# Kernel optimization log

Hardware: AMD Instinct MI355X
Metric: run time of the kernel (lower is better)

The kernel has to match this reference:

```python
import jax, jax.numpy as jnp
import numpy as np

N_NODES = 100000
N_EDGES = 1600000
D_IN, D_H, D_OUT = 256, 128, 128


def setup_inputs() -> dict:
    key = jax.random.key(0)
    ks = jax.random.split(key, 8)
    x = jax.random.normal(ks[0], (N_NODES, D_IN), dtype=jnp.float32)
    edge_index = jax.random.randint(ks[1], (2, N_EDGES), 0, N_NODES, dtype=jnp.int64)
    def glorot(k, fan_in, fan_out):
        s = jnp.sqrt(6.0 / (fan_in + fan_out))
        return jax.random.uniform(k, (fan_in, fan_out), jnp.float32, -s, s)
    W1 = glorot(ks[2], D_IN, D_H)
    b1 = jnp.zeros((D_H,), jnp.float32)
    W2 = glorot(ks[3], D_H, D_H)
    b2 = jnp.zeros((D_H,), jnp.float32)
    W3 = glorot(ks[4], D_H, D_OUT)
    b3 = jnp.zeros((D_OUT,), jnp.float32)
    return {"x": x, "edge_index": edge_index,
            "W1": W1, "b1": b1, "W2": W2, "b2": b2, "W3": W3, "b3": b3}


def _gcn_norm(edge_index, n_nodes):
    # PyG GCNConv: add self-loops, symmetric normalization D^-1/2 (A+I) D^-1/2
    loop = jnp.arange(n_nodes, dtype=edge_index.dtype)
    src = jnp.concatenate([edge_index[0], loop])  # source j
    dst = jnp.concatenate([edge_index[1], loop])  # target i
    deg = jax.ops.segment_sum(jnp.ones_like(dst, dtype=jnp.float32), dst,
                              num_segments=n_nodes)
    dinv = jnp.where(deg > 0, jax.lax.rsqrt(deg), 0.0)
    norm = dinv[src] * dinv[dst]  # [E+N]
    return src, dst, norm


def _gcn_conv(h, W, b, src, dst, norm, n_nodes):
    h = h @ W                                   # [N, d_out] transform first
    msg = h[src] * norm[:, None]                # gather + edge-weight
    out = jax.ops.segment_sum(msg, dst, num_segments=n_nodes)  # scatter-add
    return out + b


def reference(x, edge_index, W1, b1, W2, b2, W3, b3):
    n = x.shape[0]
    src, dst, norm = _gcn_norm(edge_index, n)
    h = jax.nn.relu(_gcn_conv(x, W1, b1, src, dst, norm, n))
    h = jax.nn.relu(_gcn_conv(h, W2, b2, src, dst, norm, n))
    return _gcn_conv(h, W3, b3, src, dst, norm, n)
```

## Files before the change

### kernel.cpp

```cpp
#include <hip/hip_runtime.h>
#include <hip/hip_fp16.h>
#include <math.h>


#define N_NODES 100000
#define N_EDGES 1600000
#define SLOT    56
#define NWIN    6

typedef _Float16 f16x8 __attribute__((ext_vector_type(8)));
typedef float    f32x4 __attribute__((ext_vector_type(4)));


__global__ __launch_bounds__(256) void k_init(int* __restrict__ csr, int total,
                                              int* __restrict__ cnt, int n,
                                              unsigned int* __restrict__ phz,
                                              unsigned int* __restrict__ phz2) {
    int i = blockIdx.x * 256 + threadIdx.x;
    if (i < total) csr[i] = N_NODES;
    if (i < n) cnt[i] = 0;
    if (i < 64) { phz[i] = 0; phz2[i] = 0; }
}

__global__ __launch_bounds__(256) void k_dinv(const int* __restrict__ cnt, float* __restrict__ dinv, int n) {
    int i = blockIdx.x * 256 + threadIdx.x;
    if (i < n) dinv[i] = rsqrtf((float)(cnt[i] + 1));
    else if (i == n) dinv[i] = 0.f;
}

__global__ __launch_bounds__(256) void k_wpack(const float* __restrict__ W, _Float16* __restrict__ Wpk, int K) {
    int j = blockIdx.x * 256 + threadIdx.x;
    if (j < K * 128) {
        int i  = j & 7;
        int l  = (j >> 3) & 63;
        int tc = (j >> 9) & 7;
        int c  = j >> 12;
        int col = tc * 16 + (l & 15);
        int k   = c * 32 + (l >> 4) * 8 + i;
        float w = W[(size_t)k * 128 + col];
        _Float16 h = (_Float16)w;
        Wpk[j] = h;
        Wpk[(size_t)K * 128 + j] = (_Float16)(w - (float)h);
    }
}


template <int K>
__global__ __launch_bounds__(256) void k_gemm1_fill(const float* __restrict__ X,
                                                    const _Float16* __restrict__ Wpk,
                                                    _Float16* __restrict__ Y, int n,
                                                    const int* __restrict__ src, const int* __restrict__ dst,
                                                    int* __restrict__ cnt, int* __restrict__ csr,
                                                    int E, int lo, int hi, int gemm_b0, int gemm_nb) {
    constexpr int NS = K / 64;
    __shared__ float sX[64 * 64];
    if ((int)blockIdx.x >= gemm_nb) {
        int e = (blockIdx.x - gemm_nb) * 256 + threadIdx.x;
        if (e < E) {
            int d = dst[e];
            if (d >= lo && d < hi) {
                int p = atomicAdd(&cnt[d], 1);
                csr[d * SLOT + p] = src[e];
            }
        }
        return;
    }
    const int t    = threadIdx.x;
    const int wave = t >> 6;
    const int lane = t & 63;
    const int lrow = lane & 15;
    const int kgrp = lane >> 4;
    const int row0 = (gemm_b0 + blockIdx.x) * 64;
    const int R    = wave * 16 + lrow;
    const _Float16* __restrict__ Wlo = Wpk + (size_t)K * 128;

    const int gsl = t & 15;
    const int rb  = t >> 4;
    const int r0 = rb, r1 = rb + 16, r2 = rb + 32, r3 = rb + 48;
    const int gc0 = ((gsl & 8) + ((gsl & 7) ^ (r0 & 7))) << 2;
    const int gc1 = ((gsl & 8) + ((gsl & 7) ^ (r1 & 7))) << 2;
    const int gc2 = ((gsl & 8) + ((gsl & 7) ^ (r2 & 7))) << 2;
    const int gc3 = ((gsl & 8) + ((gsl & 7) ^ (r3 & 7))) << 2;
    const bool ok0 = row0 + r0 < n, ok1 = row0 + r1 < n;
    const bool ok2 = row0 + r2 < n, ok3 = row0 + r3 < n;
    const float* __restrict__ xr0 = X + (size_t)(row0 + r0) * K;
    const float* __restrict__ xr1 = X + (size_t)(row0 + r1) * K;
    const float* __restrict__ xr2 = X + (size_t)(row0 + r2) * K;
    const float* __restrict__ xr3 = X + (size_t)(row0 + r3) * K;

    f32x4 acc[8];
    #pragma unroll
    for (int i = 0; i < 8; ++i) acc[i] = (f32x4){0.f, 0.f, 0.f, 0.f};

    const float4 z4 = make_float4(0.f, 0.f, 0.f, 0.f);
    float4 rv0 = ok0 ? *(const float4*)&xr0[gc0] : z4;
    float4 rv1 = ok1 ? *(const float4*)&xr1[gc1] : z4;
    float4 rv2 = ok2 ? *(const float4*)&xr2[gc2] : z4;
    float4 rv3 = ok3 ? *(const float4*)&xr3[gc3] : z4;
    *(float4*)&sX[(r0 * 16 + gsl) * 4] = rv0;
    *(float4*)&sX[(r1 * 16 + gsl) * 4] = rv1;
    *(float4*)&sX[(r2 * 16 + gsl) * 4] = rv2;
    *(float4*)&sX[(r3 * 16 + gsl) * 4] = rv3;
    __syncthreads();

    #pragma unroll
    for (int s = 0; s < NS; ++s) {
        if (s + 1 < NS) {
            const int o = (s + 1) * 64;
            rv0 = ok0 ? *(const float4*)&xr0[o + gc0] : z4;
            rv1 = ok1 ? *(const float4*)&xr1[o + gc1] : z4;
            rv2 = ok2 ? *(const float4*)&xr2[o + gc2] : z4;
            rv3 = ok3 ? *(const float4*)&xr3[o + gc3] : z4;
        }
        #pragma unroll
        for (int cc = 0; cc < 2; ++cc) {
            const int c = s * 2 + cc;
            float4 x0 = *(const float4*)&sX[(R * 16 + cc * 8 + ((kgrp * 2)     ^ (R & 7))) * 4];
            float4 x1 = *(const float4*)&sX[(R * 16 + cc * 8 + ((kgrp * 2 + 1) ^ (R & 7))) * 4];
            float xs[8] = {x0.x, x0.y, x0.z, x0.w, x1.x, x1.y, x1.z, x1.w};
            f16x8 ah, al;
            #pragma unroll
            for (int i = 0; i < 8; ++i) {
                _Float16 h = (_Float16)xs[i];
                ah[i] = h;
                al[i] = (_Float16)(xs[i] - (float)h);
            }
            const size_t wb = ((size_t)(c * 8) * 64 + lane) * 8;
            #pragma unroll
            for (int tc = 0; tc < 8; ++tc) {
                f16x8 bh = *(const f16x8*)(Wpk + wb + (size_t)tc * 512);
                f16x8 bl = *(const f16x8*)(Wlo + wb + (size_t)tc * 512);
                acc[tc] = __builtin_amdgcn_mfma_f32_16x16x32_f16(ah, bh, acc[tc], 0, 0, 0);
                acc[tc] = __builtin_amdgcn_mfma_f32_16x16x32_f16(al, bh, acc[tc], 0, 0, 0);
                acc[tc] = __builtin_amdgcn_mfma_f32_16x16x32_f16(ah, bl, acc[tc], 0, 0, 0);
            }
        }
        if (s + 1 < NS) {
            __syncthreads();
            *(float4*)&sX[(r0 * 16 + gsl) * 4] = rv0;
            *(float4*)&sX[(r1 * 16 + gsl) * 4] = rv1;
            *(float4*)&sX[(r2 * 16 + gsl) * 4] = rv2;
            *(float4*)&sX[(r3 * 16 + gsl) * 4] = rv3;
            __syncthreads();
        }
    }

    #pragma unroll
    for (int r = 0; r < 4; ++r) {
        int grow = row0 + wave * 16 + kgrp * 4 + r;
        if (grow < n) {
            _Float16* yr = Y + (size_t)grow * 128 + lrow;
            #pragma unroll
            for (int tc = 0; tc < 8; ++tc) yr[tc * 16] = (_Float16)acc[tc][r];
        }
    }
}


__device__ __forceinline__ void facc8(float a[8], uint4 u, float w) {
    float2 p;
    p = __half22float2(*(__half2*)&u.x); a[0] = fmaf(w, p.x, a[0]); a[1] = fmaf(w, p.y, a[1]);
    p = __half22float2(*(__half2*)&u.y); a[2] = fmaf(w, p.x, a[2]); a[3] = fmaf(w, p.y, a[3]);
    p = __half22float2(*(__half2*)&u.z); a[4] = fmaf(w, p.x, a[4]); a[5] = fmaf(w, p.y, a[5]);
    p = __half22float2(*(__half2*)&u.w); a[6] = fmaf(w, p.x, a[6]); a[7] = fmaf(w, p.y, a[7]);
}

__device__ __forceinline__ void agg_node(const uint4* __restrict__ Hu,
                                         const int* __restrict__ cnt, const int* __restrict__ csr,
                                         const float* __restrict__ dinv, const float4 b0, const float4 b1,
                                         int node, int fl, bool relu, float o[8]) {
    const float dv = dinv[node];
    float a[8];
    {
        uint4 u = Hu[(size_t)node * 16 + fl];
        float2 p;
        p = __half22float2(*(__half2*)&u.x); a[0] = dv * p.x; a[1] = dv * p.y;
        p = __half22float2(*(__half2*)&u.y); a[2] = dv * p.x; a[3] = dv * p.y;
        p = __half22float2(*(__half2*)&u.z); a[4] = dv * p.x; a[5] = dv * p.y;
        p = __half22float2(*(__half2*)&u.w); a[6] = dv * p.x; a[7] = dv * p.y;
    }
    const int c0 = node * SLOT;
    const int cn = cnt[node];
    for (int e8 = 0; e8 < cn; e8 += 8) {
        const int4* qp = (const int4*)(csr + c0 + e8);
        int4 qa = qp[0], qb = qp[1];
        uint4 u0 = Hu[(size_t)qa.x * 16 + fl];
        uint4 u1 = Hu[(size_t)qa.y * 16 + fl];
        uint4 u2 = Hu[(size_t)qa.z * 16 + fl];
        uint4 u3 = Hu[(size_t)qa.w * 16 + fl];
        uint4 u4 = Hu[(size_t)qb.x * 16 + fl];
        uint4 u5 = Hu[(size_t)qb.y * 16 + fl];
        uint4 u6 = Hu[(size_t)qb.z * 16 + fl];
        uint4 u7 = Hu[(size_t)qb.w * 16 + fl];
        float d0 = dinv[qa.x], d1 = dinv[qa.y], d2 = dinv[qa.z], d3 = dinv[qa.w];
        float d4 = dinv[qb.x], d5 = dinv[qb.y], d6 = dinv[qb.z], d7 = dinv[qb.w];
        facc8(a, u0, d0); facc8(a, u1, d1); facc8(a, u2, d2); facc8(a, u3, d3);
        facc8(a, u4, d4); facc8(a, u5, d5); facc8(a, u6, d6); facc8(a, u7, d7);
    }
    o[0] = fmaf(dv, a[0], b0.x); o[1] = fmaf(dv, a[1], b0.y);
    o[2] = fmaf(dv, a[2], b0.z); o[3] = fmaf(dv, a[3], b0.w);
    o[4] = fmaf(dv, a[4], b1.x); o[5] = fmaf(dv, a[5], b1.y);
    o[6] = fmaf(dv, a[6], b1.z); o[7] = fmaf(dv, a[7], b1.w);
    if (relu) {
        #pragma unroll
        for (int i = 0; i < 8; ++i) o[i] = fmaxf(o[i], 0.f);
    }
}


__global__ __launch_bounds__(256) void k_agg_gemm(const __half* __restrict__ H,
                                                  const int* __restrict__ cnt, const int* __restrict__ csr,
                                                  const float* __restrict__ dinv,
                                                  const float* __restrict__ bias,
                                                  const _Float16* __restrict__ Wpk,
                                                  _Float16* __restrict__ Y, int n) {
    constexpr int K = 128;
    __shared__ unsigned int sQ[64 * 68];
    const int t    = threadIdx.x;
    const int wave = t >> 6;
    const int lane = t & 63;
    const int q    = lane >> 4;
    const int fl   = lane & 15;
    const int row0 = blockIdx.x * 64;
    const uint4* __restrict__ Hu = (const uint4*)H;
    const float4 b0 = *(const float4*)&bias[fl * 8];
    const float4 b1 = *(const float4*)&bias[fl * 8 + 4];

    #pragma unroll
    for (int p = 0; p < 4; ++p) {
        const int lr   = wave * 16 + p * 4 + q;
        const int node = row0 + lr;
        float o[8] = {0.f, 0.f, 0.f, 0.f, 0.f, 0.f, 0.f, 0.f};
        if (node < n)
            agg_node(Hu, cnt, csr, dinv, b0, b1, node, fl, true, o);
        f16x8 hv;
        #pragma unroll
        for (int i = 0; i < 8; ++i) hv[i] = (_Float16)o[i];
        *(uint4*)&sQ[lr * 68 + fl * 4] = *(uint4*)&hv;
    }

    const int lrow = lane & 15;
    const int kgrp = lane >> 4;
    const _Float16* __restrict__ Wlo = Wpk + (size_t)K * 128;
    f32x4 acc[8];
    #pragma unroll
    for (int i = 0; i < 8; ++i) acc[i] = (f32x4){0.f, 0.f, 0.f, 0.f};

    #pragma unroll
    for (int c = 0; c < K / 32; ++c) {
        f16x8 a = *(const f16x8*)&sQ[(wave * 16 + lrow) * 68 + c * 16 + kgrp * 4];
        const size_t wb = ((size_t)(c * 8) * 64 + lane) * 8;
        #pragma unroll
        for (int tc = 0; tc < 8; ++tc) {
            f16x8 bh = *(const f16x8*)(Wpk + wb + (size_t)tc * 512);
            f16x8 bl = *(const f16x8*)(Wlo + wb + (size_t)tc * 512);
            acc[tc] = __builtin_amdgcn_mfma_f32_16x16x32_f16(a, bh, acc[tc], 0, 0, 0);
            acc[tc] = __builtin_amdgcn_mfma_f32_16x16x32_f16(a, bl, acc[tc], 0, 0, 0);
        }
    }

    #pragma unroll
    for (int r = 0; r < 4; ++r) {
        int grow = row0 + wave * 16 + kgrp * 4 + r;
        if (grow < n) {
            _Float16* yr = Y + (size_t)grow * 128 + lrow;
            #pragma unroll
            for (int tc = 0; tc < 8; ++tc) yr[tc * 16] = (_Float16)acc[tc][r];
        }
    }
}


__global__ __launch_bounds__(256) void k_agg_final(const __half* __restrict__ H,
                                                   const int* __restrict__ cnt, const int* __restrict__ csr,
                                                   const float* __restrict__ dinv, const float* __restrict__ bias,
                                                   float* __restrict__ out, int n) {
    const int lane  = threadIdx.x & 63;
    const int q     = lane >> 4;
    const int fl    = lane & 15;
    const int wave0 = (int)((blockIdx.x * 256 + threadIdx.x) >> 6);
    const int nwave = (int)((gridDim.x * 256) >> 6);
    const uint4* __restrict__ Hu = (const uint4*)H;
    const float4 b0 = *(const float4*)&bias[fl * 8];
    const float4 b1 = *(const float4*)&bias[fl * 8 + 4];

    const int nquad = n >> 2;
    for (int g = wave0; g < nquad; g += nwave) {
        const int node = g * 4 + q;
        float o[8];
        agg_node(Hu, cnt, csr, dinv, b0, b1, node, fl, false, o);
        float* op = out + (size_t)node * 128 + fl * 8;
        *(float4*)&op[0] = make_float4(o[0], o[1], o[2], o[3]);
        *(float4*)&op[4] = make_float4(o[4], o[5], o[6], o[7]);
    }
}


extern "C" void kernel_launch(void* const* d_in, const int* in_sizes, int n_in,
                              void* d_out, int out_size, void* d_ws, size_t ws_size,
                              hipStream_t stream) {
    const float* x  = (const float*)d_in[0];
    const int*   ei = (const int*)d_in[1];
    const float* W1 = (const float*)d_in[2];
    const float* b1 = (const float*)d_in[3];
    const float* W2 = (const float*)d_in[4];
    const float* b2 = (const float*)d_in[5];
    const float* W3 = (const float*)d_in[6];
    const float* b3 = (const float*)d_in[7];
    float* out = (float*)d_out;

    const int N = N_NODES, E = N_EDGES;
    const int* src = ei;
    const int* dst = ei + E;

    char* w = (char*)d_ws;
    auto alloc = [&](size_t bytes) -> void* {
        void* p = (void*)w;
        w += (bytes + 255) & ~(size_t)255;
        return p;
    };
    int*      cnt  = (int*)alloc((size_t)N * 4);
    float*    dinv = (float*)alloc((size_t)(N + 8) * 4);
    int*      csr  = (int*)alloc((size_t)N * SLOT * 4);
    _Float16* Ph   = (_Float16*)alloc((size_t)(N + 8) * 128 * 2);
    _Float16* Ph2  = (_Float16*)alloc((size_t)(N + 8) * 128 * 2);
    _Float16* Wpk1 = (_Float16*)alloc((size_t)2 * 256 * 128 * 2);
    _Float16* Wpk2 = (_Float16*)alloc((size_t)2 * 128 * 128 * 2);
    _Float16* Wpk3 = (_Float16*)alloc((size_t)2 * 128 * 128 * 2);

    const int nbE = (E + 255) / 256;
    const int total_slots = N * SLOT;
    const int nbI = (total_slots + 255) / 256;
    const int gemm_grid = (N + 63) / 64;
    const int agg_grid  = 2048;

    k_init<<<nbI, 256, 0, stream>>>(csr, total_slots, cnt, N,
                                    (unsigned int*)(Ph + (size_t)N * 128),
                                    (unsigned int*)(Ph2 + (size_t)N * 128));
    k_wpack<<<(256 * 128 + 255) / 256, 256, 0, stream>>>(W1, Wpk1, 256);
    k_wpack<<<(128 * 128 + 255) / 256, 256, 0, stream>>>(W2, Wpk2, 128);
    k_wpack<<<(128 * 128 + 255) / 256, 256, 0, stream>>>(W3, Wpk3, 128);

    const int win   = (N + NWIN - 1) / NWIN;
    const int slice = (gemm_grid + NWIN - 1) / NWIN;
    for (int p = 0; p < NWIN; ++p) {
        int lo = p * win;
        int hi = (p == NWIN - 1) ? N : (p + 1) * win;
        int gb0 = p * slice;
        int gnb = gemm_grid - gb0; if (gnb > slice) gnb = slice; if (gnb < 0) gnb = 0;
        k_gemm1_fill<256><<<gnb + nbE, 256, 0, stream>>>(x, Wpk1, Ph, N, src, dst,
                                                         cnt, csr, E, lo, hi, gb0, gnb);
    }

    k_dinv<<<(N + 256) / 256 + 1, 256, 0, stream>>>(cnt, dinv, N);

    k_agg_gemm<<<gemm_grid, 256, 0, stream>>>((const __half*)Ph,  cnt, csr, dinv, b1, Wpk2, Ph2, N);
    k_agg_gemm<<<gemm_grid, 256, 0, stream>>>((const __half*)Ph2, cnt, csr, dinv, b2, Wpk3, Ph,  N);
    k_agg_final<<<agg_grid, 256, 0, stream>>>((const __half*)Ph, cnt, csr, dinv, b3, out, N);
}
```

Baseline: 378.9 us.

## Pre-scale GEMM outputs by dinv to drop per-edge dinv gathers; grid-stride CSR fill

The agg-gemm kernels now multiply each output row by dinv before storing, so the next aggregation can sum neighbour features unweighted and skip eight dinv gathers and FMAs per edge chunk. The first aggregation stays weighted because layer-1 GEMM output is not pre-scaled. Separately, the CSR fill part of the first-layer kernel uses a fixed 2048-block grid-stride loop instead of one block per 256 edges for each of the six windows, cutting launched blocks. Pre-scaling before fp16 storage changes rounding slightly.

```diff
diff --git a/kernel.cpp b/kernel.cpp
--- a/kernel.cpp
+++ b/kernel.cpp
@@ -7,6 +7,7 @@
 #define N_EDGES 1600000
 #define SLOT    56
 #define NWIN    6
+#define NBF     2048
 
 typedef _Float16 f16x8 __attribute__((ext_vector_type(8)));
 typedef float    f32x4 __attribute__((ext_vector_type(4)));
@@ -55,8 +56,8 @@
     constexpr int NS = K / 64;
     __shared__ float sX[64 * 64];
     if ((int)blockIdx.x >= gemm_nb) {
-        int e = (blockIdx.x - gemm_nb) * 256 + threadIdx.x;
-        if (e < E) {
+        const int nf = gridDim.x - gemm_nb;
+        for (int e = (blockIdx.x - gemm_nb) * 256 + threadIdx.x; e < E; e += nf * 256) {
             int d = dst[e];
             if (d >= lo && d < hi) {
                 int p = atomicAdd(&cnt[d], 1);
@@ -165,6 +166,15 @@
     p = __half22float2(*(__half2*)&u.w); a[6] = fmaf(w, p.x, a[6]); a[7] = fmaf(w, p.y, a[7]);
 }
 
+__device__ __forceinline__ void acc8(float a[8], uint4 u) {
+    float2 p;
+    p = __half22float2(*(__half2*)&u.x); a[0] += p.x; a[1] += p.y;
+    p = __half22float2(*(__half2*)&u.y); a[2] += p.x; a[3] += p.y;
+    p = __half22float2(*(__half2*)&u.z); a[4] += p.x; a[5] += p.y;
+    p = __half22float2(*(__half2*)&u.w); a[6] += p.x; a[7] += p.y;
+}
+
+template <bool WEIGHTED>
 __device__ __forceinline__ void agg_node(const uint4* __restrict__ Hu,
                                          const int* __restrict__ cnt, const int* __restrict__ csr,
                                          const float* __restrict__ dinv, const float4 b0, const float4 b1,
@@ -173,11 +183,12 @@
     float a[8];
     {
         uint4 u = Hu[(size_t)node * 16 + fl];
+        const float s = WEIGHTED ? dv : 1.f;
         float2 p;
-        p = __half22float2(*(__half2*)&u.x); a[0] = dv * p.x; a[1] = dv * p.y;
-        p = __half22float2(*(__half2*)&u.y); a[2] = dv * p.x; a[3] = dv * p.y;
-        p = __half22float2(*(__half2*)&u.z); a[4] = dv * p.x; a[5] = dv * p.y;
-        p = __half22float2(*(__half2*)&u.w); a[6] = dv * p.x; a[7] = dv * p.y;
+        p = __half22float2(*(__half2*)&u.x); a[0] = s * p.x; a[1] = s * p.y;
+        p = __half22float2(*(__half2*)&u.y); a[2] = s * p.x; a[3] = s * p.y;
+        p = __half22float2(*(__half2*)&u.z); a[4] = s * p.x; a[5] = s * p.y;
+        p = __half22float2(*(__half2*)&u.w); a[6] = s * p.x; a[7] = s * p.y;
     }
     const int c0 = node * SLOT;
     const int cn = cnt[node];
@@ -192,10 +203,15 @@
         uint4 u5 = Hu[(size_t)qb.y * 16 + fl];
         uint4 u6 = Hu[(size_t)qb.z * 16 + fl];
         uint4 u7 = Hu[(size_t)qb.w * 16 + fl];
-        float d0 = dinv[qa.x], d1 = dinv[qa.y], d2 = dinv[qa.z], d3 = dinv[qa.w];
-        float d4 = dinv[qb.x], d5 = dinv[qb.y], d6 = dinv[qb.z], d7 = dinv[qb.w];
-        facc8(a, u0, d0); facc8(a, u1, d1); facc8(a, u2, d2); facc8(a, u3, d3);
-        facc8(a, u4, d4); facc8(a, u5, d5); facc8(a, u6, d6); facc8(a, u7, d7);
+        if (WEIGHTED) {
+            float d0 = dinv[qa.x], d1 = dinv[qa.y], d2 = dinv[qa.z], d3 = dinv[qa.w];
+            float d4 = dinv[qb.x], d5 = dinv[qb.y], d6 = dinv[qb.z], d7 = dinv[qb.w];
+            facc8(a, u0, d0); facc8(a, u1, d1); facc8(a, u2, d2); facc8(a, u3, d3);
+            facc8(a, u4, d4); facc8(a, u5, d5); facc8(a, u6, d6); facc8(a, u7, d7);
+        } else {
+            acc8(a, u0); acc8(a, u1); acc8(a, u2); acc8(a, u3);
+            acc8(a, u4); acc8(a, u5); acc8(a, u6); acc8(a, u7);
+        }
     }
     o[0] = fmaf(dv, a[0], b0.x); o[1] = fmaf(dv, a[1], b0.y);
     o[2] = fmaf(dv, a[2], b0.z); o[3] = fmaf(dv, a[3], b0.w);
@@ -208,6 +224,7 @@
 }
 
 
+template <bool WEIGHTED>
 __global__ __launch_bounds__(256) void k_agg_gemm(const __half* __restrict__ H,
                                                   const int* __restrict__ cnt, const int* __restrict__ csr,
                                                   const float* __restrict__ dinv,
@@ -232,7 +249,7 @@
         const int node = row0 + lr;
         float o[8] = {0.f, 0.f, 0.f, 0.f, 0.f, 0.f, 0.f, 0.f};
         if (node < n)
-            agg_node(Hu, cnt, csr, dinv, b0, b1, node, fl, true, o);
+            agg_node<WEIGHTED>(Hu, cnt, csr, dinv, b0, b1, node, fl, true, o);
         f16x8 hv;
         #pragma unroll
         for (int i = 0; i < 8; ++i) hv[i] = (_Float16)o[i];
@@ -263,9 +280,10 @@
     for (int r = 0; r < 4; ++r) {
         int grow = row0 + wave * 16 + kgrp * 4 + r;
         if (grow < n) {
+            float dv = dinv[grow];
             _Float16* yr = Y + (size_t)grow * 128 + lrow;
             #pragma unroll
-            for (int tc = 0; tc < 8; ++tc) yr[tc * 16] = (_Float16)acc[tc][r];
+            for (int tc = 0; tc < 8; ++tc) yr[tc * 16] = (_Float16)(dv * acc[tc][r]);
         }
     }
 }
@@ -288,7 +306,7 @@
     for (int g = wave0; g < nquad; g += nwave) {
         const int node = g * 4 + q;
         float o[8];
-        agg_node(Hu, cnt, csr, dinv, b0, b1, node, fl, false, o);
+        agg_node<false>(Hu, cnt, csr, dinv, b0, b1, node, fl, false, o);
         float* op = out + (size_t)node * 128 + fl * 8;
         *(float4*)&op[0] = make_float4(o[0], o[1], o[2], o[3]);
         *(float4*)&op[4] = make_float4(o[4], o[5], o[6], o[7]);
@@ -328,7 +346,6 @@
     _Float16* Wpk2 = (_Float16*)alloc((size_t)2 * 128 * 128 * 2);
     _Float16* Wpk3 = (_Float16*)alloc((size_t)2 * 128 * 128 * 2);
 
-    const int nbE = (E + 255) / 256;
     const int total_slots = N * SLOT;
     const int nbI = (total_slots + 255) / 256;
     const int gemm_grid = (N + 63) / 64;
@@ -348,13 +365,13 @@
         int hi = (p == NWIN - 1) ? N : (p + 1) * win;
         int gb0 = p * slice;
         int gnb = gemm_grid - gb0; if (gnb > slice) gnb = slice; if (gnb < 0) gnb = 0;
-        k_gemm1_fill<256><<<gnb + nbE, 256, 0, stream>>>(x, Wpk1, Ph, N, src, dst,
+        k_gemm1_fill<256><<<gnb + NBF, 256, 0, stream>>>(x, Wpk1, Ph, N, src, dst,
                                                          cnt, csr, E, lo, hi, gb0, gnb);
     }
 
     k_dinv<<<(N + 256) / 256 + 1, 256, 0, stream>>>(cnt, dinv, N);
 
-    k_agg_gemm<<<gemm_grid, 256, 0, stream>>>((const __half*)Ph,  cnt, csr, dinv, b1, Wpk2, Ph2, N);
-    k_agg_gemm<<<gemm_grid, 256, 0, stream>>>((const __half*)Ph2, cnt, csr, dinv, b2, Wpk3, Ph,  N);
+    k_agg_gemm<true ><<<gemm_grid, 256, 0, stream>>>((const __half*)Ph,  cnt, csr, dinv, b1, Wpk2, Ph2, N);
+    k_agg_gemm<false><<<gemm_grid, 256, 0, stream>>>((const __half*)Ph2, cnt, csr, dinv, b2, Wpk3, Ph,  N);
     k_agg_final<<<agg_grid, 256, 0, stream>>>((const __half*)Ph, cnt, csr, dinv, b3, out, N);
 }
```

After: 396.0 us. 1.05x slower.
